# Kernel tuning notes

Measured on AMD Instinct MI355X. Metric: run time of the kernel, lower is better.

## Reference

```python
import jax, jax.numpy as jnp
import numpy as np

D = 1024
H = 16
DH = D // H
MAX_TYPES = 256
B, L = 8, 1024
EPS = 1e-5


def setup_inputs() -> dict:
    key = jax.random.key(0)
    ks = jax.random.split(key, 16)
    s = 0.02
    return {
        'type_ids': jax.random.randint(ks[0], (B, L), 0, MAX_TYPES),
        'values': jax.random.normal(ks[1], (B, L, 1), jnp.float32),
        'deltas': jax.random.uniform(ks[2], (B, L, 1), jnp.float32),
        'type_emb': jax.random.normal(ks[3], (MAX_TYPES, D), jnp.float32) * s,
        'Wv': jax.random.normal(ks[4], (D, 1), jnp.float32) * s,
        'bv': jnp.zeros((D,), jnp.float32),
        'Wt': jax.random.normal(ks[5], (D, 1), jnp.float32) * s,
        'bt': jnp.zeros((D,), jnp.float32),
        'Win': jax.random.normal(ks[6], (3 * D, D), jnp.float32) * s,
        'bin': jnp.zeros((3 * D,), jnp.float32),
        'Wout': jax.random.normal(ks[7], (D, D), jnp.float32) * s,
        'bout': jnp.zeros((D,), jnp.float32),
        'W1': jax.random.normal(ks[8], (D, D), jnp.float32) * s,
        'b1': jnp.zeros((D,), jnp.float32),
        'W2': jax.random.normal(ks[9], (D, D), jnp.float32) * s,
        'b2': jnp.zeros((D,), jnp.float32),
        'gamma': jnp.ones((D,), jnp.float32),
        'beta': jnp.zeros((D,), jnp.float32),
    }


def _ln(x, gamma, beta):
    mu = jnp.mean(x, axis=-1, keepdims=True)
    var = jnp.mean(jnp.square(x - mu), axis=-1, keepdims=True)
    return (x - mu) * jax.lax.rsqrt(var + EPS) * gamma + beta


def reference(type_ids, values, deltas, type_emb, Wv, bv, Wt, bt,
              Win, bin, Wout, bout, W1, b1, W2, b2, gamma, beta):
    # fused embedding: type lookup + value/time linear projections
    h = type_emb[type_ids] + values @ Wv.T + bv + deltas @ Wt.T + bt  # [B,L,D]
    b, l, d = h.shape
    # multi-head self-attention (explicit weights path, need_weights=True)
    qkv = h @ Win.T + bin  # [B,L,3D]
    q, k, v = jnp.split(qkv, 3, axis=-1)
    q = q.reshape(b, l, H, DH)
    k = k.reshape(b, l, H, DH)
    v = v.reshape(b, l, H, DH)
    scale = 1.0 / jnp.sqrt(jnp.asarray(DH, h.dtype))
    scores = jnp.einsum('blhd,bmhd->bhlm', q, k) * scale  # [B,H,L,L]
    w = jax.nn.softmax(scores, axis=-1)
    attn = jnp.einsum('bhlm,bmhd->blhd', w, v).reshape(b, l, d)
    attn_out = attn @ Wout.T + bout
    h2 = _ln(h + attn_out, gamma, beta)
    ff = jax.nn.relu(h2 @ W1.T + b1) @ W2.T + b2
    h3 = _ln(h2 + ff, gamma, beta)
    pooled = h3.mean(axis=1)  # [B,D]
    attn_tokens = w.mean(axis=1).mean(axis=2)  # mean over heads, then keys -> [B,L]
    return pooled, attn_tokens
```

## Files before the change

### kernel.cpp

```cpp
#include <hip/hip_runtime.h>
#include <hip/hip_bf16.h>


#define Dm 1024
#define Hh 16
#define Bb 8
#define Ll 1024
#define Mm 8192
#define LNEPS 1e-5f

typedef __attribute__((ext_vector_type(8))) short s16x8;
typedef __attribute__((ext_vector_type(4))) short s16x4;
typedef __attribute__((ext_vector_type(4))) float f32x4;

using bf16 = __hip_bfloat16;

__device__ __forceinline__ short f2bs(float f) {
  return __builtin_bit_cast(short, __float2bfloat16(f));
}

__device__ __forceinline__ unsigned cvtpk(float lo, float hi) {
  unsigned r;
  asm("v_cvt_pk_bf16_f32 %0, %1, %2" : "=v"(r) : "v"(lo), "v"(hi));
  return r;
}

__device__ __forceinline__ void gload16(const void* g, void* l) {
  __builtin_amdgcn_global_load_lds(
      (__attribute__((address_space(1))) void*)g,
      (__attribute__((address_space(3))) void*)l, 16, 0, 0);
}

__global__ __launch_bounds__(256) void k_f2b(const float* __restrict__ x, bf16* __restrict__ y)
{
  const size_t i = ((size_t)blockIdx.x * 256 + threadIdx.x) * 4;
  const float4 v = *(const float4*)&x[i];
  s16x4 o;
  o[0] = f2bs(v.x); o[1] = f2bs(v.y); o[2] = f2bs(v.z); o[3] = f2bs(v.w);
  *(s16x4*)&y[i] = o;
}

__global__ __launch_bounds__(256) void k_embed(
    const int* __restrict__ tids, const float* __restrict__ vals, const float* __restrict__ dels,
    const float* __restrict__ temb, const float* __restrict__ Wv, const float* __restrict__ bv,
    const float* __restrict__ Wt, const float* __restrict__ bt,
    float* __restrict__ hf, bf16* __restrict__ hb)
{
  const int row = blockIdx.x;
  const int ty = tids[row];
  const float v = vals[row], dl = dels[row];
  const int d0 = threadIdx.x * 4;
  const float4 e  = *(const float4*)&temb[(size_t)ty * Dm + d0];
  const float4 wv = *(const float4*)&Wv[d0];
  const float4 c1 = *(const float4*)&bv[d0];
  const float4 wt = *(const float4*)&Wt[d0];
  const float4 c2 = *(const float4*)&bt[d0];
  float4 h;
  h.x = e.x + v * wv.x + c1.x + dl * wt.x + c2.x;
  h.y = e.y + v * wv.y + c1.y + dl * wt.y + c2.y;
  h.z = e.z + v * wv.z + c1.z + dl * wt.z + c2.z;
  h.w = e.w + v * wv.w + c1.w + dl * wt.w + c2.w;
  *(float4*)&hf[(size_t)row * Dm + d0] = h;
  s16x4 o;
  o[0] = f2bs(h.x); o[1] = f2bs(h.y); o[2] = f2bs(h.z); o[3] = f2bs(h.w);
  *(s16x4*)((short*)hb + (size_t)row * Dm + d0) = o;
}

template<bool RELU, bool OUTF, bool OUTB, bool RES>
__global__ __launch_bounds__(512) void k_gemm8(
    const bf16* __restrict__ A, const bf16* __restrict__ Bt,
    const float* __restrict__ bias, const float* __restrict__ res,
    float* __restrict__ outF, bf16* __restrict__ outB, const int N, const int K)
{
  __shared__ __attribute__((aligned(16))) short lds[49152];
  const int tid = threadIdx.x, lane = tid & 63, wave = tid >> 6;
  const int wr = wave >> 2, wc = wave & 3;
  const int l15 = lane & 15, lg = (lane >> 4) & 3;
  const int bm = blockIdx.x, bn = blockIdx.y;
  const int NT = K >> 6;

  const int rl = tid >> 3;
  const int swz = ((tid & 7) ^ (rl & 7)) * 8;
  const bf16* aSrc = A  + (size_t)(bm * 128 + rl) * K + swz;
  const bf16* bSrc = Bt + (size_t)(bn * 256 + rl) * K + swz;

  f32x4 acc[4][4] = {};

  auto stageA = [&](int t, int h) {
    gload16(aSrc + (size_t)h * 64 * K + t * 64,
            &lds[(t & 1) * 24576 + h * 4096 + tid * 8]);
  };
  auto stageB = [&](int t, int h) {
    gload16(bSrc + (size_t)h * 128 * K + t * 64,
            &lds[(t & 1) * 24576 + 8192 + h * 8192 + tid * 8]);
    gload16(bSrc + (size_t)(h * 128 + 64) * K + t * 64,
            &lds[(t & 1) * 24576 + 8192 + h * 8192 + 4096 + tid * 8]);
  };

  stageA(0, 0); stageA(0, 1); stageB(0, 0); stageB(0, 1);
  if (NT > 1) { stageA(1, 0); stageA(1, 1); }
  asm volatile("s_waitcnt vmcnt(2)" ::: "memory");
  __builtin_amdgcn_sched_barrier(0);
  __builtin_amdgcn_s_barrier();

  for (int t = 0; t < NT; ++t) {
    const int cb = (t & 1) * 24576;
    s16x8 fa[4][2], fb[2][2];

#pragma unroll
    for (int m = 0; m < 4; ++m)
#pragma unroll
      for (int ks = 0; ks < 2; ++ks) {
        const int row = wr * 64 + m * 16 + l15;
        fa[m][ks] = *(const s16x8*)&lds[cb + row * 64 + (((ks * 4 + lg) ^ (row & 7)) << 3)];
      }
#pragma unroll
    for (int n = 0; n < 2; ++n)
#pragma unroll
      for (int ks = 0; ks < 2; ++ks) {
        const int row = wc * 64 + n * 16 + l15;
        fb[n][ks] = *(const s16x8*)&lds[cb + 8192 + row * 64 + (((ks * 4 + lg) ^ (row & 7)) << 3)];
      }
    if (t + 1 < NT) { stageB(t + 1, 0); stageB(t + 1, 1); }
    __builtin_amdgcn_s_barrier();
    asm volatile("s_waitcnt lgkmcnt(0)" ::: "memory");
    __builtin_amdgcn_sched_barrier(0);
    __builtin_amdgcn_s_setprio(1);
#pragma unroll
    for (int m = 0; m < 4; ++m)
#pragma unroll
      for (int n = 0; n < 2; ++n)
#pragma unroll
        for (int ks = 0; ks < 2; ++ks)
          acc[m][n] = __builtin_amdgcn_mfma_f32_16x16x32_bf16(fa[m][ks], fb[n][ks], acc[m][n], 0, 0, 0);
    __builtin_amdgcn_s_setprio(0);
    __builtin_amdgcn_s_barrier();

#pragma unroll
    for (int n = 0; n < 2; ++n)
#pragma unroll
      for (int ks = 0; ks < 2; ++ks) {
        const int row = wc * 64 + (2 + n) * 16 + l15;
        fb[n][ks] = *(const s16x8*)&lds[cb + 8192 + row * 64 + (((ks * 4 + lg) ^ (row & 7)) << 3)];
      }
    if (t + 2 < NT) { stageA(t + 2, 0); stageA(t + 2, 1); }
    __builtin_amdgcn_s_barrier();
    asm volatile("s_waitcnt lgkmcnt(0)" ::: "memory");
    __builtin_amdgcn_sched_barrier(0);
    __builtin_amdgcn_s_setprio(1);
#pragma unroll
    for (int m = 0; m < 4; ++m)
#pragma unroll
      for (int n = 0; n < 2; ++n)
#pragma unroll
        for (int ks = 0; ks < 2; ++ks)
          acc[m][2 + n] = __builtin_amdgcn_mfma_f32_16x16x32_bf16(fa[m][ks], fb[n][ks], acc[m][2 + n], 0, 0, 0);
    __builtin_amdgcn_s_setprio(0);

    if (t + 1 < NT) {
      if (t + 2 < NT) asm volatile("s_waitcnt vmcnt(2)" ::: "memory");
      else            asm volatile("s_waitcnt vmcnt(0)" ::: "memory");
      __builtin_amdgcn_sched_barrier(0);
      __builtin_amdgcn_s_barrier();
    }
  }

#pragma unroll
  for (int n = 0; n < 4; ++n) {
    const int col = bn * 256 + wc * 64 + n * 16 + l15;
    const float bc = bias[col];
#pragma unroll
    for (int m = 0; m < 4; ++m) {
#pragma unroll
      for (int i = 0; i < 4; ++i) {
        const size_t row = (size_t)bm * 128 + wr * 64 + m * 16 + lg * 4 + i;
        float v = acc[m][n][i] + bc;
        if constexpr (RES)  v += res[row * N + col];
        if constexpr (RELU) v = fmaxf(v, 0.f);
        if constexpr (OUTF) outF[row * N + col] = v;
        if constexpr (OUTB) outB[row * N + col] = __float2bfloat16(v);
      }
    }
  }
}

__global__ __launch_bounds__(256) void k_vt(const bf16* __restrict__ qkv, bf16* __restrict__ vt)
{
  const int bh = blockIdx.x, lc = blockIdx.y;
  const int b = bh >> 4, h = bh & 15;
  __shared__ short tile[64][72];
  const int r = threadIdx.x >> 2;
  const int c0 = (threadIdx.x & 3) << 4;
  const short* src = (const short*)qkv + ((size_t)(b * Ll + lc * 64 + r)) * 3072 + 2048 + h * 64 + c0;
  const s16x8 x0 = *(const s16x8*)src;
  const s16x8 x1 = *(const s16x8*)(src + 8);
#pragma unroll
  for (int j = 0; j < 8; ++j) { tile[r][c0 + j] = x0[j]; tile[r][c0 + 8 + j] = x1[j]; }
  __syncthreads();
  s16x8 y0, y1;
#pragma unroll
  for (int j = 0; j < 8; ++j) { y0[j] = tile[c0 + j][r]; y1[j] = tile[c0 + 8 + j][r]; }
  short* dst = (short*)vt + ((size_t)(bh * 64 + r)) * Ll + lc * 64 + c0;
  *(s16x8*)dst = y0;
  *(s16x8*)(dst + 8) = y1;
}

__global__ __launch_bounds__(256) void k_attn(
    const bf16* __restrict__ qkv, const bf16* __restrict__ vt, bf16* __restrict__ attnb)
{
  const int bh = blockIdx.x;
  const int qb = blockIdx.y;
  const int b = bh >> 4, h = bh & 15;
  __shared__ __attribute__((aligned(16))) short lK[4096];
  __shared__ __attribute__((aligned(16))) short lV[4096];
  __shared__ __attribute__((aligned(16))) short lP[8192];
  const int tid = threadIdx.x, lane = tid & 63, wave = tid >> 6;
  const int l15 = lane & 15, lg = lane >> 4;
  const int qrow = wave * 32;
  const int l7 = l15 & 7;

  s16x8 qf[2][2];
#pragma unroll
  for (int mq = 0; mq < 2; ++mq)
#pragma unroll
    for (int ks = 0; ks < 2; ++ks)
      qf[mq][ks] = *(const s16x8*)((const short*)qkv +
          ((size_t)(b * Ll + qb * 128 + qrow + mq * 16 + l15)) * 3072 + h * 64 + ks * 32 + lg * 8);

  f32x4 o[2][4] = {};
  float rs[2] = {0.f, 0.f};

  const int sr = tid >> 3;
  const int swz = (tid & 7) ^ (sr & 7);

  for (int mc = 0; mc < 16; ++mc) {
    __syncthreads();
    {
      const bf16* gk = qkv + ((size_t)(b * Ll + mc * 64 + sr)) * 3072 + 1024 + h * 64 + swz * 8;
      gload16(gk,                     &lK[tid * 8]);
      gload16(gk + (size_t)32 * 3072, &lK[2048 + tid * 8]);
      const bf16* gv = vt + ((size_t)(bh * 64 + sr)) * Ll + mc * 64 + swz * 8;
      gload16(gv,                   &lV[tid * 8]);
      gload16(gv + (size_t)32 * Ll, &lV[2048 + tid * 8]);
    }
    __syncthreads();

    f32x4 st[2][4] = {};
    __builtin_amdgcn_s_setprio(1);
#pragma unroll
    for (int ks = 0; ks < 2; ++ks) {
#pragma unroll
      for (int n = 0; n < 4; ++n) {
        const int kr = n * 16 + l15;
        const s16x8 kf = *(const s16x8*)&lK[kr * 64 + (((ks * 4 + lg) ^ l7) << 3)];
        st[0][n] = __builtin_amdgcn_mfma_f32_16x16x32_bf16(kf, qf[0][ks], st[0][n], 0, 0, 0);
        st[1][n] = __builtin_amdgcn_mfma_f32_16x16x32_bf16(kf, qf[1][ks], st[1][n], 0, 0, 0);
      }
    }
    __builtin_amdgcn_s_setprio(0);

#pragma unroll
    for (int mq = 0; mq < 2; ++mq) {
      const int qr = qrow + mq * 16 + l15;
      short* prow = &lP[qr * 64];
      float loc = 0.f;
#pragma unroll
      for (int n = 0; n < 4; ++n) {
        const float e0 = __expf(st[mq][n][0] * 0.125f);
        const float e1 = __expf(st[mq][n][1] * 0.125f);
        const float e2 = __expf(st[mq][n][2] * 0.125f);
        const float e3 = __expf(st[mq][n][3] * 0.125f);
        loc += (e0 + e1) + (e2 + e3);
        const unsigned c0 = cvtpk(e0, e1);
        const unsigned c1 = cvtpk(e2, e3);
        const int col0 = n * 16 + lg * 4;
        const int scol = ((((col0 >> 3) ^ (qr & 7)) << 3) | (col0 & 7));
        *(unsigned*)&prow[scol]     = c0;
        *(unsigned*)&prow[scol + 2] = c1;
      }
      rs[mq] += loc;
    }

    __builtin_amdgcn_s_setprio(1);
#pragma unroll
    for (int ks = 0; ks < 2; ++ks) {
      s16x8 pa[2];
#pragma unroll
      for (int mq = 0; mq < 2; ++mq) {
        const int qr = qrow + mq * 16 + l15;
        pa[mq] = *(const s16x8*)&lP[qr * 64 + (((ks * 4 + lg) ^ (qr & 7)) << 3)];
      }
#pragma unroll
      for (int dn = 0; dn < 4; ++dn) {
        const int vr = dn * 16 + l15;
        const s16x8 vf = *(const s16x8*)&lV[vr * 64 + (((ks * 4 + lg) ^ l7) << 3)];
        o[0][dn] = __builtin_amdgcn_mfma_f32_16x16x32_bf16(pa[0], vf, o[0][dn], 0, 0, 0);
        o[1][dn] = __builtin_amdgcn_mfma_f32_16x16x32_bf16(pa[1], vf, o[1][dn], 0, 0, 0);
      }
    }
    __builtin_amdgcn_s_setprio(0);
  }

#pragma unroll
  for (int mq = 0; mq < 2; ++mq) {
    rs[mq] += __shfl_xor(rs[mq], 16);
    rs[mq] += __shfl_xor(rs[mq], 32);
  }
#pragma unroll
  for (int mq = 0; mq < 2; ++mq) {
    float inv[4];
#pragma unroll
    for (int i = 0; i < 4; ++i)
      inv[i] = 1.f / __shfl(rs[mq], lg * 4 + i);
#pragma unroll
    for (int dn = 0; dn < 4; ++dn) {
#pragma unroll
      for (int i = 0; i < 4; ++i) {
        const int q = qb * 128 + qrow + mq * 16 + lg * 4 + i;
        attnb[((size_t)(b * Ll + q)) * Dm + h * 64 + dn * 16 + l15] =
            __float2bfloat16(o[mq][dn][i] * inv[i]);
      }
    }
  }
}

template<bool WB>
__global__ __launch_bounds__(256) void k_ln(const float* __restrict__ x,
    const float* __restrict__ gamma, const float* __restrict__ beta,
    float* __restrict__ yf, bf16* __restrict__ yb)
{
  const size_t row = blockIdx.x;
  const int d0 = threadIdx.x * 4;
  const float4 xv = *(const float4*)&x[row * Dm + d0];
  float s  = xv.x + xv.y + xv.z + xv.w;
  float ss = xv.x * xv.x + xv.y * xv.y + xv.z * xv.z + xv.w * xv.w;
#pragma unroll
  for (int m = 1; m < 64; m <<= 1) { s += __shfl_xor(s, m); ss += __shfl_xor(ss, m); }
  __shared__ float red[8];
  const int wv = threadIdx.x >> 6;
  if ((threadIdx.x & 63) == 0) { red[wv] = s; red[4 + wv] = ss; }
  __syncthreads();
  s  = red[0] + red[1] + red[2] + red[3];
  ss = red[4] + red[5] + red[6] + red[7];
  const float mu = s * (1.f / Dm);
  const float rstd = rsqrtf(ss * (1.f / Dm) - mu * mu + LNEPS);
  const float4 g  = *(const float4*)&gamma[d0];
  const float4 be = *(const float4*)&beta[d0];
  float4 y;
  y.x = (xv.x - mu) * rstd * g.x + be.x;
  y.y = (xv.y - mu) * rstd * g.y + be.y;
  y.z = (xv.z - mu) * rstd * g.z + be.z;
  y.w = (xv.w - mu) * rstd * g.w + be.w;
  *(float4*)&yf[row * Dm + d0] = y;
  if constexpr (WB) {
    s16x4 o;
    o[0] = f2bs(y.x); o[1] = f2bs(y.y); o[2] = f2bs(y.z); o[3] = f2bs(y.w);
    *(s16x4*)((short*)yb + row * Dm + d0) = o;
  }
}

__global__ __launch_bounds__(256) void k_pool_part(const float* __restrict__ h3, float* __restrict__ part)
{
  const int b = blockIdx.x, lcn = blockIdx.y, dz = blockIdx.z;
  const int d = dz * 256 + threadIdx.x;
  float s = 0.f;
#pragma unroll 4
  for (int l = 0; l < 64; ++l)
    s += h3[((size_t)(b * Ll + lcn * 64 + l)) * Dm + d];
  part[((size_t)(b * 16 + lcn)) * Dm + d] = s;
}

__global__ __launch_bounds__(256) void k_pool_fin(const float* __restrict__ part, float* __restrict__ out)
{
  const int b = blockIdx.x;
  const int d = blockIdx.y * 256 + threadIdx.x;
  float s = 0.f;
#pragma unroll
  for (int c = 0; c < 16; ++c) s += part[((size_t)(b * 16 + c)) * Dm + d];
  out[b * Dm + d] = s * (1.f / Ll);
  out[(size_t)Mm + b * Dm + d] = 1.f / Ll;
}

extern "C" void kernel_launch(void* const* d_in, const int* in_sizes, int n_in,
                              void* d_out, int out_size, void* d_ws, size_t ws_size,
                              hipStream_t stream) {
  const int*   tids  = (const int*)  d_in[0];
  const float* vals  = (const float*)d_in[1];
  const float* dels  = (const float*)d_in[2];
  const float* temb  = (const float*)d_in[3];
  const float* Wv    = (const float*)d_in[4];
  const float* bv    = (const float*)d_in[5];
  const float* Wt    = (const float*)d_in[6];
  const float* bt    = (const float*)d_in[7];
  const float* Win   = (const float*)d_in[8];
  const float* bin   = (const float*)d_in[9];
  const float* Wout  = (const float*)d_in[10];
  const float* bout  = (const float*)d_in[11];
  const float* W1    = (const float*)d_in[12];
  const float* b1    = (const float*)d_in[13];
  const float* W2    = (const float*)d_in[14];
  const float* b2    = (const float*)d_in[15];
  const float* gamma = (const float*)d_in[16];
  const float* beta  = (const float*)d_in[17];
  float* out = (float*)d_out;

  char* w = (char*)d_ws;
  const size_t MB = 1ull << 20;
  float* hf    = (float*)(w + 0);
  bf16*  hb    = (bf16*) (w + 32 * MB);
  bf16*  qkv   = (bf16*) (w + 48 * MB);
  bf16*  vtb   = (bf16*) (w + 96 * MB);
  bf16*  attnb = (bf16*) (w + 112 * MB);
  float* x1    = (float*)(w + 48 * MB);
  float* h2f   = (float*)(w + 80 * MB);
  bf16*  h2b   = (bf16*) (w + 32 * MB);
  bf16*  ff1   = (bf16*) (w + 112 * MB);
  float* x2    = (float*)(w + 0);
  float* h3    = (float*)(w + 48 * MB);
  bf16*  WinB  = (bf16*) (w + 129 * MB);
  bf16*  WoutB = (bf16*) (w + 135 * MB);
  bf16*  W1B   = (bf16*) (w + 137 * MB);
  bf16*  W2B   = (bf16*) (w + 139 * MB);
  float* part  = (float*)(w + 141 * MB);

  k_f2b<<<3072, 256, 0, stream>>>(Win,  WinB);
  k_f2b<<<1024, 256, 0, stream>>>(Wout, WoutB);
  k_f2b<<<1024, 256, 0, stream>>>(W1,   W1B);
  k_f2b<<<1024, 256, 0, stream>>>(W2,   W2B);

  k_embed<<<Mm, 256, 0, stream>>>(tids, vals, dels, temb, Wv, bv, Wt, bt, hf, hb);

  k_gemm8<false, false, true, false><<<dim3(64, 12), 512, 0, stream>>>(
      hb, WinB, bin, nullptr, nullptr, qkv, 3072, 1024);

  k_vt<<<dim3(128, 16), 256, 0, stream>>>(qkv, vtb);
  k_attn<<<dim3(128, 8), 256, 0, stream>>>(qkv, vtb, attnb);

  k_gemm8<false, true, false, true><<<dim3(64, 4), 512, 0, stream>>>(
      attnb, WoutB, bout, hf, x1, nullptr, 1024, 1024);

  k_ln<true><<<Mm, 256, 0, stream>>>(x1, gamma, beta, h2f, h2b);

  k_gemm8<true, false, true, false><<<dim3(64, 4), 512, 0, stream>>>(
      h2b, W1B, b1, nullptr, nullptr, ff1, 1024, 1024);

  k_gemm8<false, true, false, true><<<dim3(64, 4), 512, 0, stream>>>(
      ff1, W2B, b2, h2f, x2, nullptr, 1024, 1024);

  k_ln<false><<<Mm, 256, 0, stream>>>(x2, gamma, beta, h3, nullptr);

  k_pool_part<<<dim3(8, 16, 4), 256, 0, stream>>>(h3, part);
  k_pool_fin<<<dim3(8, 4), 256, 0, stream>>>(part, out);
}
```

Measured before the change: 257.2 us.

## Store residual and layernorm activations in bf16, merge weight casts, double-buffer attention K/V

All fp32 intermediate activations (embedding output, residual sums, layernorm outputs, h3) become bf16 only. This removes the fp32 stores and reloads in the embed, GEMM epilogues, layernorm and pooling stages. The four weight-conversion launches are merged into one kernel. The attention kernel double-buffers its K/V tiles in LDS so the next chunk's load overlaps the current compute. The cost is lower precision on the residual path and the layernorm inputs.

```diff
diff --git a/kernel.cpp b/kernel.cpp
--- a/kernel.cpp
+++ b/kernel.cpp
@@ -18,6 +18,9 @@
 __device__ __forceinline__ short f2bs(float f) {
   return __builtin_bit_cast(short, __float2bfloat16(f));
 }
+__device__ __forceinline__ float b2f(short s) {
+  return __builtin_bit_cast(float, ((unsigned)(unsigned short)s) << 16);
+}
 
 __device__ __forceinline__ unsigned cvtpk(float lo, float hi) {
   unsigned r;
@@ -31,20 +34,30 @@
       (__attribute__((address_space(3))) void*)l, 16, 0, 0);
 }
 
-__global__ __launch_bounds__(256) void k_f2b(const float* __restrict__ x, bf16* __restrict__ y)
-{
-  const size_t i = ((size_t)blockIdx.x * 256 + threadIdx.x) * 4;
-  const float4 v = *(const float4*)&x[i];
+__global__ __launch_bounds__(256) void k_f2b4(
+    const float* __restrict__ w0, const float* __restrict__ w1,
+    const float* __restrict__ w2, const float* __restrict__ w3,
+    bf16* __restrict__ o0, bf16* __restrict__ o1,
+    bf16* __restrict__ o2, bf16* __restrict__ o3)
+{
+  const int bId = blockIdx.x;
+  const float* src; bf16* dst; int rel;
+  if (bId < 3072)      { src = w0; dst = o0; rel = bId; }
+  else if (bId < 4096) { src = w1; dst = o1; rel = bId - 3072; }
+  else if (bId < 5120) { src = w2; dst = o2; rel = bId - 4096; }
+  else                 { src = w3; dst = o3; rel = bId - 5120; }
+  const size_t i = ((size_t)rel * 256 + threadIdx.x) * 4;
+  const float4 v = *(const float4*)&src[i];
   s16x4 o;
   o[0] = f2bs(v.x); o[1] = f2bs(v.y); o[2] = f2bs(v.z); o[3] = f2bs(v.w);
-  *(s16x4*)&y[i] = o;
+  *(s16x4*)&dst[i] = o;
 }
 
 __global__ __launch_bounds__(256) void k_embed(
     const int* __restrict__ tids, const float* __restrict__ vals, const float* __restrict__ dels,
     const float* __restrict__ temb, const float* __restrict__ Wv, const float* __restrict__ bv,
     const float* __restrict__ Wt, const float* __restrict__ bt,
-    float* __restrict__ hf, bf16* __restrict__ hb)
+    bf16* __restrict__ hb)
 {
   const int row = blockIdx.x;
   const int ty = tids[row];
@@ -55,22 +68,19 @@
   const float4 c1 = *(const float4*)&bv[d0];
   const float4 wt = *(const float4*)&Wt[d0];
   const float4 c2 = *(const float4*)&bt[d0];
-  float4 h;
-  h.x = e.x + v * wv.x + c1.x + dl * wt.x + c2.x;
-  h.y = e.y + v * wv.y + c1.y + dl * wt.y + c2.y;
-  h.z = e.z + v * wv.z + c1.z + dl * wt.z + c2.z;
-  h.w = e.w + v * wv.w + c1.w + dl * wt.w + c2.w;
-  *(float4*)&hf[(size_t)row * Dm + d0] = h;
   s16x4 o;
-  o[0] = f2bs(h.x); o[1] = f2bs(h.y); o[2] = f2bs(h.z); o[3] = f2bs(h.w);
+  o[0] = f2bs(e.x + v * wv.x + c1.x + dl * wt.x + c2.x);
+  o[1] = f2bs(e.y + v * wv.y + c1.y + dl * wt.y + c2.y);
+  o[2] = f2bs(e.z + v * wv.z + c1.z + dl * wt.z + c2.z);
+  o[3] = f2bs(e.w + v * wv.w + c1.w + dl * wt.w + c2.w);
   *(s16x4*)((short*)hb + (size_t)row * Dm + d0) = o;
 }
 
-template<bool RELU, bool OUTF, bool OUTB, bool RES>
+template<bool RELU, bool RES>
 __global__ __launch_bounds__(512) void k_gemm8(
     const bf16* __restrict__ A, const bf16* __restrict__ Bt,
-    const float* __restrict__ bias, const float* __restrict__ res,
-    float* __restrict__ outF, bf16* __restrict__ outB, const int N, const int K)
+    const float* __restrict__ bias, const bf16* __restrict__ res,
+    bf16* __restrict__ outB, const int N, const int K)
 {
   __shared__ __attribute__((aligned(16))) short lds[49152];
   const int tid = threadIdx.x, lane = tid & 63, wave = tid >> 6;
@@ -175,10 +185,9 @@
       for (int i = 0; i < 4; ++i) {
         const size_t row = (size_t)bm * 128 + wr * 64 + m * 16 + lg * 4 + i;
         float v = acc[m][n][i] + bc;
-        if constexpr (RES)  v += res[row * N + col];
+        if constexpr (RES)  v += b2f(((const short*)res)[row * N + col]);
         if constexpr (RELU) v = fmaxf(v, 0.f);
-        if constexpr (OUTF) outF[row * N + col] = v;
-        if constexpr (OUTB) outB[row * N + col] = __float2bfloat16(v);
+        outB[row * N + col] = __float2bfloat16(v);
       }
     }
   }
@@ -211,8 +220,8 @@
   const int bh = blockIdx.x;
   const int qb = blockIdx.y;
   const int b = bh >> 4, h = bh & 15;
-  __shared__ __attribute__((aligned(16))) short lK[4096];
-  __shared__ __attribute__((aligned(16))) short lV[4096];
+  __shared__ __attribute__((aligned(16))) short lK[8192];
+  __shared__ __attribute__((aligned(16))) short lV[8192];
   __shared__ __attribute__((aligned(16))) short lP[8192];
   const int tid = threadIdx.x, lane = tid & 63, wave = tid >> 6;
   const int l15 = lane & 15, lg = lane >> 4;
@@ -233,17 +242,24 @@
   const int sr = tid >> 3;
   const int swz = (tid & 7) ^ (sr & 7);
 
+  auto stage = [&](int mc) {
+    const int bo = (mc & 1) * 4096;
+    const bf16* gk = qkv + ((size_t)(b * Ll + mc * 64 + sr)) * 3072 + 1024 + h * 64 + swz * 8;
+    gload16(gk,                     &lK[bo + tid * 8]);
+    gload16(gk + (size_t)32 * 3072, &lK[bo + 2048 + tid * 8]);
+    const bf16* gv = vt + ((size_t)(bh * 64 + sr)) * Ll + mc * 64 + swz * 8;
+    gload16(gv,                   &lV[bo + tid * 8]);
+    gload16(gv + (size_t)32 * Ll, &lV[bo + 2048 + tid * 8]);
+  };
+
+  stage(0);
+
   for (int mc = 0; mc < 16; ++mc) {
-    __syncthreads();
-    {
-      const bf16* gk = qkv + ((size_t)(b * Ll + mc * 64 + sr)) * 3072 + 1024 + h * 64 + swz * 8;
-      gload16(gk,                     &lK[tid * 8]);
-      gload16(gk + (size_t)32 * 3072, &lK[2048 + tid * 8]);
-      const bf16* gv = vt + ((size_t)(bh * 64 + sr)) * Ll + mc * 64 + swz * 8;
-      gload16(gv,                   &lV[tid * 8]);
-      gload16(gv + (size_t)32 * Ll, &lV[2048 + tid * 8]);
-    }
-    __syncthreads();
+    asm volatile("s_waitcnt vmcnt(0)" ::: "memory");
+    __builtin_amdgcn_s_barrier();
+    __builtin_amdgcn_sched_barrier(0);
+    if (mc + 1 < 16) stage(mc + 1);
+    const int bo = (mc & 1) * 4096;
 
     f32x4 st[2][4] = {};
     __builtin_amdgcn_s_setprio(1);
@@ -252,7 +268,7 @@
 #pragma unroll
       for (int n = 0; n < 4; ++n) {
         const int kr = n * 16 + l15;
-        const s16x8 kf = *(const s16x8*)&lK[kr * 64 + (((ks * 4 + lg) ^ l7) << 3)];
+        const s16x8 kf = *(const s16x8*)&lK[bo + kr * 64 + (((ks * 4 + lg) ^ l7) << 3)];
         st[0][n] = __builtin_amdgcn_mfma_f32_16x16x32_bf16(kf, qf[0][ks], st[0][n], 0, 0, 0);
         st[1][n] = __builtin_amdgcn_mfma_f32_16x16x32_bf16(kf, qf[1][ks], st[1][n], 0, 0, 0);
       }
@@ -293,12 +309,13 @@
 #pragma unroll
       for (int dn = 0; dn < 4; ++dn) {
         const int vr = dn * 16 + l15;
-        const s16x8 vf = *(const s16x8*)&lV[vr * 64 + (((ks * 4 + lg) ^ l7) << 3)];
+        const s16x8 vf = *(const s16x8*)&lV[bo + vr * 64 + (((ks * 4 + lg) ^ l7) << 3)];
         o[0][dn] = __builtin_amdgcn_mfma_f32_16x16x32_bf16(pa[0], vf, o[0][dn], 0, 0, 0);
         o[1][dn] = __builtin_amdgcn_mfma_f32_16x16x32_bf16(pa[1], vf, o[1][dn], 0, 0, 0);
       }
     }
     __builtin_amdgcn_s_setprio(0);
+    asm volatile("s_waitcnt lgkmcnt(0)" ::: "memory");
   }
 
 #pragma unroll
@@ -324,16 +341,16 @@
   }
 }
 
-template<bool WB>
-__global__ __launch_bounds__(256) void k_ln(const float* __restrict__ x,
+__global__ __launch_bounds__(256) void k_ln(const bf16* __restrict__ x,
     const float* __restrict__ gamma, const float* __restrict__ beta,
-    float* __restrict__ yf, bf16* __restrict__ yb)
+    bf16* __restrict__ y)
 {
   const size_t row = blockIdx.x;
   const int d0 = threadIdx.x * 4;
-  const float4 xv = *(const float4*)&x[row * Dm + d0];
-  float s  = xv.x + xv.y + xv.z + xv.w;
-  float ss = xv.x * xv.x + xv.y * xv.y + xv.z * xv.z + xv.w * xv.w;
+  const s16x4 xv = *(const s16x4*)((const short*)x + row * Dm + d0);
+  float f0 = b2f(xv[0]), f1 = b2f(xv[1]), f2 = b2f(xv[2]), f3 = b2f(xv[3]);
+  float s  = (f0 + f1) + (f2 + f3);
+  float ss = (f0 * f0 + f1 * f1) + (f2 * f2 + f3 * f3);
 #pragma unroll
   for (int m = 1; m < 64; m <<= 1) { s += __shfl_xor(s, m); ss += __shfl_xor(ss, m); }
   __shared__ float red[8];
@@ -346,27 +363,22 @@
   const float rstd = rsqrtf(ss * (1.f / Dm) - mu * mu + LNEPS);
   const float4 g  = *(const float4*)&gamma[d0];
   const float4 be = *(const float4*)&beta[d0];
-  float4 y;
-  y.x = (xv.x - mu) * rstd * g.x + be.x;
-  y.y = (xv.y - mu) * rstd * g.y + be.y;
-  y.z = (xv.z - mu) * rstd * g.z + be.z;
-  y.w = (xv.w - mu) * rstd * g.w + be.w;
-  *(float4*)&yf[row * Dm + d0] = y;
-  if constexpr (WB) {
-    s16x4 o;
-    o[0] = f2bs(y.x); o[1] = f2bs(y.y); o[2] = f2bs(y.z); o[3] = f2bs(y.w);
-    *(s16x4*)((short*)yb + row * Dm + d0) = o;
-  }
-}
-
-__global__ __launch_bounds__(256) void k_pool_part(const float* __restrict__ h3, float* __restrict__ part)
+  s16x4 o;
+  o[0] = f2bs((f0 - mu) * rstd * g.x + be.x);
+  o[1] = f2bs((f1 - mu) * rstd * g.y + be.y);
+  o[2] = f2bs((f2 - mu) * rstd * g.z + be.z);
+  o[3] = f2bs((f3 - mu) * rstd * g.w + be.w);
+  *(s16x4*)((short*)y + row * Dm + d0) = o;
+}
+
+__global__ __launch_bounds__(256) void k_pool_part(const bf16* __restrict__ h3, float* __restrict__ part)
 {
   const int b = blockIdx.x, lcn = blockIdx.y, dz = blockIdx.z;
   const int d = dz * 256 + threadIdx.x;
   float s = 0.f;
 #pragma unroll 4
   for (int l = 0; l < 64; ++l)
-    s += h3[((size_t)(b * Ll + lcn * 64 + l)) * Dm + d];
+    s += b2f(((const short*)h3)[((size_t)(b * Ll + lcn * 64 + l)) * Dm + d]);
   part[((size_t)(b * 16 + lcn)) * Dm + d] = s;
 }
 
@@ -406,49 +418,44 @@
 
   char* w = (char*)d_ws;
   const size_t MB = 1ull << 20;
-  float* hf    = (float*)(w + 0);
-  bf16*  hb    = (bf16*) (w + 32 * MB);
-  bf16*  qkv   = (bf16*) (w + 48 * MB);
-  bf16*  vtb   = (bf16*) (w + 96 * MB);
-  bf16*  attnb = (bf16*) (w + 112 * MB);
-  float* x1    = (float*)(w + 48 * MB);
-  float* h2f   = (float*)(w + 80 * MB);
+  bf16*  hb    = (bf16*) (w + 0);
+  bf16*  qkv   = (bf16*) (w + 16 * MB);
+  bf16*  vtb   = (bf16*) (w + 64 * MB);
+  bf16*  attnb = (bf16*) (w + 80 * MB);
+  bf16*  x1b   = (bf16*) (w + 16 * MB);
   bf16*  h2b   = (bf16*) (w + 32 * MB);
-  bf16*  ff1   = (bf16*) (w + 112 * MB);
-  float* x2    = (float*)(w + 0);
-  float* h3    = (float*)(w + 48 * MB);
-  bf16*  WinB  = (bf16*) (w + 129 * MB);
-  bf16*  WoutB = (bf16*) (w + 135 * MB);
-  bf16*  W1B   = (bf16*) (w + 137 * MB);
-  bf16*  W2B   = (bf16*) (w + 139 * MB);
-  float* part  = (float*)(w + 141 * MB);
-
-  k_f2b<<<3072, 256, 0, stream>>>(Win,  WinB);
-  k_f2b<<<1024, 256, 0, stream>>>(Wout, WoutB);
-  k_f2b<<<1024, 256, 0, stream>>>(W1,   W1B);
-  k_f2b<<<1024, 256, 0, stream>>>(W2,   W2B);
-
-  k_embed<<<Mm, 256, 0, stream>>>(tids, vals, dels, temb, Wv, bv, Wt, bt, hf, hb);
-
-  k_gemm8<false, false, true, false><<<dim3(64, 12), 512, 0, stream>>>(
-      hb, WinB, bin, nullptr, nullptr, qkv, 3072, 1024);
+  bf16*  ff1   = (bf16*) (w + 48 * MB);
+  bf16*  x2b   = (bf16*) (w + 64 * MB);
+  bf16*  h3b   = (bf16*) (w + 80 * MB);
+  bf16*  WinB  = (bf16*) (w + 96 * MB);
+  bf16*  WoutB = (bf16*) (w + 102 * MB);
+  bf16*  W1B   = (bf16*) (w + 104 * MB);
+  bf16*  W2B   = (bf16*) (w + 106 * MB);
+  float* part  = (float*)(w + 108 * MB);
+
+  k_f2b4<<<6144, 256, 0, stream>>>(Win, Wout, W1, W2, WinB, WoutB, W1B, W2B);
+
+  k_embed<<<Mm, 256, 0, stream>>>(tids, vals, dels, temb, Wv, bv, Wt, bt, hb);
+
+  k_gemm8<false, false><<<dim3(64, 12), 512, 0, stream>>>(
+      hb, WinB, bin, nullptr, qkv, 3072, 1024);
 
   k_vt<<<dim3(128, 16), 256, 0, stream>>>(qkv, vtb);
   k_attn<<<dim3(128, 8), 256, 0, stream>>>(qkv, vtb, attnb);
 
-  k_gemm8<false, true, false, true><<<dim3(64, 4), 512, 0, stream>>>(
-      attnb, WoutB, bout, hf, x1, nullptr, 1024, 1024);
-
-  k_ln<true><<<Mm, 256, 0, stream>>>(x1, gamma, beta, h2f, h2b);
-
-  k_gemm8<true, false, true, false><<<dim3(64, 4), 512, 0, stream>>>(
-      h2b, W1B, b1, nullptr, nullptr, ff1, 1024, 1024);
-
-  k_gemm8<false, true, false, true><<<dim3(64, 4), 512, 0, stream>>>(
-      ff1, W2B, b2, h2f, x2, nullptr, 1024, 1024);
-
-  k_ln<false><<<Mm, 256, 0, stream>>>(x2, gamma, beta, h3, nullptr);
-
-  k_pool_part<<<dim3(8, 16, 4), 256, 0, stream>>>(h3, part);
+  k_gemm8<false, true><<<dim3(64, 4), 512, 0, stream>>>(
+      attnb, WoutB, bout, hb, x1b, 1024, 1024);
+
+  k_ln<<<Mm, 256, 0, stream>>>(x1b, gamma, beta, h2b);
+
+  k_gemm8<true, false><<<dim3(64, 4), 512, 0, stream>>>(
+      h2b, W1B, b1, nullptr, ff1, 1024, 1024);
+
+  k_gemm8<false, true><<<dim3(64, 4), 512, 0, stream>>>(
+      ff1, W2B, b2, h2b, x2b, 1024, 1024);
+
+  k_ln<<<Mm, 256, 0, stream>>>(x2b, gamma, beta, h3b);
+
+  k_pool_part<<<dim3(8, 16, 4), 256, 0, stream>>>(h3b, part);
   k_pool_fin<<<dim3(8, 4), 256, 0, stream>>>(part, out);
 }
```

Measured after the change: 242.7 us. 5.6% less time.
